# Performance work log

Hardware: AMD Instinct MI355X
Metric: run time of the kernel (lower is better)

Reference implementation:

```python
import jax, jax.numpy as jnp
import numpy as np

HEAD_DIM = 64  # config['head_dim']
# dropout_prob=0.1 is a no-op in eval mode; reference computes deterministic attention.

def setup_inputs() -> dict:
    key = jax.random.key(0)
    kq, kk, kv = jax.random.split(key, 3)
    shape = (2, 12, 2048, HEAD_DIM)  # [batch, heads, seq, head_dim]
    Q = jax.random.normal(kq, shape, dtype=jnp.float32)
    K = jax.random.normal(kk, shape, dtype=jnp.float32)
    V = jax.random.normal(kv, shape, dtype=jnp.float32)
    return {"Q": Q, "K": K, "V": V}

def reference(Q, K, V):
    # dot = Q @ K^T / sqrt(head_dim); attn = softmax(dot); X = attn @ V
    scale = 1.0 / np.float32(np.sqrt(HEAD_DIM))
    dot = jnp.einsum('bhqd,bhkd->bhqk', Q, K) * scale  # [B,H,S,S]
    attn = jax.nn.softmax(dot, axis=-1)
    X = jnp.einsum('bhqk,bhkd->bhqd', attn, V)
    return X
```

## Files before the change

kernel.cpp:

```cpp
#include <hip/hip_runtime.h>
#include <hip/hip_bf16.h>

typedef __attribute__((ext_vector_type(8))) short bf16x8;
typedef __attribute__((ext_vector_type(4))) float f32x4;
typedef __attribute__((ext_vector_type(4))) unsigned short u16x4;
typedef __attribute__((ext_vector_type(2))) unsigned int u32x2;
typedef __attribute__((ext_vector_type(4))) unsigned int u32x4;
typedef __attribute__((ext_vector_type(4))) _Float16 f16x4;
typedef __attribute__((ext_vector_type(8))) _Float16 f16x8;
typedef __attribute__((ext_vector_type(2))) __fp16 h16x2;
typedef __attribute__((ext_vector_type(4))) __fp16 h16x4;

#define SEQ 2048
#define HD 64
#define BH 24

__device__ __forceinline__ unsigned bfpack(float a, float b) {
  union { float f; unsigned u; } ua, ub; ua.f = a; ub.f = b;
  return __builtin_amdgcn_perm(ub.u + 0x8000u, ua.u + 0x8000u, 0x07060302u);
}
__device__ __forceinline__ unsigned short f2bf(float f) {
  union { float f; unsigned u; } v; v.f = f;
  unsigned r = v.u + 0x7fffu + ((v.u >> 16) & 1u);
  return (unsigned short)(r >> 16);
}

__global__ __launch_bounds__(256) void prep_kv(const float* __restrict__ K,
                                               const float* __restrict__ V,
                                               unsigned* __restrict__ Kb,
                                               _Float16* __restrict__ Vt) {
  __shared__ _Float16 t[64 * 68];
  const int bh = blockIdx.y;
  const int k0 = blockIdx.x * 64;
  const int tid = threadIdx.x;

  const float4* ks = (const float4*)(K + ((size_t)bh * SEQ + k0) * HD);
  unsigned* kd = Kb + ((size_t)bh * SEQ + k0) * (HD / 2);
#pragma unroll
  for (int i = 0; i < 4; ++i) {
    int f = tid + i * 256;
    float4 v = ks[f];
    u32x2 o;
    o.x = bfpack(v.x, v.y);
    o.y = bfpack(v.z, v.w);
    *(u32x2*)&kd[f * 2] = o;
  }

  const float4* vs = (const float4*)(V + ((size_t)bh * SEQ + k0) * HD);
#pragma unroll
  for (int i = 0; i < 4; ++i) {
    int f = tid + i * 256;
    int k = f >> 4, cg = f & 15;
    float4 v = vs[k * 16 + cg];
    int dg = cg * 4;
    t[(dg + 0) * 68 + k] = (_Float16)v.x;
    t[(dg + 1) * 68 + k] = (_Float16)v.y;
    t[(dg + 2) * 68 + k] = (_Float16)v.z;
    t[(dg + 3) * 68 + k] = (_Float16)v.w;
  }
  __syncthreads();
  int d = tid >> 2, kg = (tid & 3) * 16;
  _Float16* g = Vt + ((size_t)(bh * 64 + d)) * SEQ + k0 + (kg & 32) + ((kg >> 4) & 1) * 4;
#pragma unroll
  for (int r = 0; r < 4; ++r) {
    f16x4 x = *(f16x4*)&t[d * 68 + kg + r * 4];
    *(f16x4*)&g[r * 8] = x;
  }
}

__global__ __launch_bounds__(128) void attn_main(const float* __restrict__ Q,
                                                 const unsigned short* __restrict__ Kb,
                                                 const _Float16* __restrict__ Vt,
                                                 float* __restrict__ O) {
  __shared__ unsigned short kv[2][8192];

  const int tid  = threadIdx.x;
  const int lane = tid & 63;
  const int wv   = tid >> 6;
  const int quad = lane >> 4;
  const int n    = lane & 15;

  const int bh = blockIdx.x;
  const int q0 = blockIdx.y * 64;

  const float qscale = 0.125f * 1.44269504088896f;

  bf16x8 qf[2][2];
#pragma unroll
  for (int u = 0; u < 2; ++u) {
    const float* qb = Q + ((size_t)bh * SEQ + q0 + wv * 32 + u * 16 + n) * HD;
#pragma unroll
    for (int h = 0; h < 2; ++h) {
      float4 a = *(const float4*)(qb + h * 32 + quad * 8);
      float4 b = *(const float4*)(qb + h * 32 + quad * 8 + 4);
      u32x4 pk;
      pk.x = bfpack(a.x * qscale, a.y * qscale);
      pk.y = bfpack(a.z * qscale, a.w * qscale);
      pk.z = bfpack(b.x * qscale, b.y * qscale);
      pk.w = bfpack(b.z * qscale, b.w * qscale);
      qf[u][h] = __builtin_bit_cast(bf16x8, pk);
    }
  }

  const unsigned short* Kbase = Kb + (size_t)bh * SEQ * HD;
  const unsigned short* Vbase = (const unsigned short*)(Vt + (size_t)bh * HD * SEQ);
  const unsigned short* ksrc[4];
  const unsigned short* vsrc[4];
  int soff[4];
#pragma unroll
  for (int i = 0; i < 4; ++i) {
    int s = i * 128 + tid;
    int r = s >> 3, p = s & 7, G = p ^ (r & 7);
    ksrc[i] = Kbase + r * HD + G * 8;
    vsrc[i] = Vbase + (size_t)r * SEQ + G * 8;
    soff[i] = s * 8;
  }

#define DMA(it_)                                                                          \
  {                                                                                       \
    unsigned short* db_ = &kv[(it_) & 1][0];                                              \
    _Pragma("unroll")                                                                     \
    for (int i_ = 0; i_ < 4; ++i_) {                                                      \
      __builtin_amdgcn_global_load_lds(                                                   \
          (const __attribute__((address_space(1))) void*)(ksrc[i_] + (size_t)(it_) * 4096), \
          (__attribute__((address_space(3))) void*)(db_ + soff[i_]), 16, 0, 0);           \
      __builtin_amdgcn_global_load_lds(                                                   \
          (const __attribute__((address_space(1))) void*)(vsrc[i_] + (size_t)(it_) * 64), \
          (__attribute__((address_space(3))) void*)(db_ + 4096 + soff[i_]), 16, 0, 0);    \
    }                                                                                     \
  }

  f32x4 o[2][4] = {{{0,0,0,0},{0,0,0,0},{0,0,0,0},{0,0,0,0}},
                   {{0,0,0,0},{0,0,0,0},{0,0,0,0},{0,0,0,0}}};
  float lsum[2] = {0.f, 0.f};

  int ro[2];
#pragma unroll
  for (int h = 0; h < 2; ++h) ro[h] = n * 64 + (((h * 4 + quad) ^ (n & 7)) * 8);

  DMA(0);

  for (int it = 0; it < 32; ++it) {
    __syncthreads();
    if (it + 1 < 32) DMA(it + 1);

    const unsigned short* kb = &kv[it & 1][0];
    const unsigned short* vb = kb + 4096;

    f32x4 s[2][4] = {{{0,0,0,0},{0,0,0,0},{0,0,0,0},{0,0,0,0}},
                     {{0,0,0,0},{0,0,0,0},{0,0,0,0},{0,0,0,0}}};
#pragma unroll
    for (int t = 0; t < 4; ++t) {
#pragma unroll
      for (int h = 0; h < 2; ++h) {
        bf16x8 a = *(const bf16x8*)&kb[t * 1024 + ro[h]];
#pragma unroll
        for (int u = 0; u < 2; ++u)
          s[u][t] = __builtin_amdgcn_mfma_f32_16x16x32_bf16(a, qf[u][h], s[u][t], 0, 0, 0);
      }
    }

    f16x4 pf[2][4];
#pragma unroll
    for (int u = 0; u < 2; ++u) {
#pragma unroll
      for (int c = 0; c < 4; ++c) {
        float e0 = __builtin_amdgcn_exp2f(s[u][c][0]);
        float e1 = __builtin_amdgcn_exp2f(s[u][c][1]);
        float e2 = __builtin_amdgcn_exp2f(s[u][c][2]);
        float e3 = __builtin_amdgcn_exp2f(s[u][c][3]);
        lsum[u] += (e0 + e1) + (e2 + e3);
        h16x2 a_ = __builtin_amdgcn_cvt_pkrtz(e0, e1);
        h16x2 b_ = __builtin_amdgcn_cvt_pkrtz(e2, e3);
        h16x4 ab_ = __builtin_shufflevector(a_, b_, 0, 1, 2, 3);
        pf[u][c] = __builtin_bit_cast(f16x4, ab_);
      }
    }

#pragma unroll
    for (int t = 0; t < 4; ++t) {
#pragma unroll
      for (int h = 0; h < 2; ++h) {
        f16x8 v8 = *(const f16x8*)((const _Float16*)&vb[t * 1024 + ro[h]]);
        f16x4 vlo = __builtin_shufflevector(v8, v8, 0, 1, 2, 3);
        f16x4 vhi = __builtin_shufflevector(v8, v8, 4, 5, 6, 7);
#pragma unroll
        for (int u = 0; u < 2; ++u) {
          o[u][t] = __builtin_amdgcn_mfma_f32_16x16x16f16(vlo, pf[u][2 * h], o[u][t], 0, 0, 0);
          o[u][t] = __builtin_amdgcn_mfma_f32_16x16x16f16(vhi, pf[u][2 * h + 1], o[u][t], 0, 0, 0);
        }
      }
    }
  }
#undef DMA

#pragma unroll
  for (int u = 0; u < 2; ++u) {
    float l = lsum[u];
    l += __shfl_xor(l, 16);
    l += __shfl_xor(l, 32);
    float inv = 1.0f / l;
    float* og = O + ((size_t)bh * SEQ + q0 + wv * 32 + u * 16 + n) * HD + quad * 4;
#pragma unroll
    for (int t = 0; t < 4; ++t) {
      f32x4 r = o[u][t];
      r.x *= inv; r.y *= inv; r.z *= inv; r.w *= inv;
      *(f32x4*)(og + t * 16) = r;
    }
  }
}

#define F_QT 128
#define F_KT 64
#define F_LD 72

__global__ __launch_bounds__(512) void attn_fwd(const float* __restrict__ Q,
                                                const float* __restrict__ K,
                                                const float* __restrict__ V,
                                                float* __restrict__ O) {
  __shared__ unsigned short sm[(F_QT + F_KT + HD + 8 * 16) * F_LD];
  unsigned short* Qs = sm;
  unsigned short* Ks = Qs + F_QT * F_LD;
  unsigned short* Vt = Ks + F_KT * F_LD;
  unsigned short* Ps = Vt + HD * F_LD;

  const int tid = threadIdx.x, lane = tid & 63, wv = tid >> 6;
  const int quad = lane >> 4, n = lane & 15;
  const int bh = blockIdx.y, q0 = blockIdx.x * F_QT;
  const float* Qg = Q + ((size_t)bh * SEQ + q0) * HD;
  const float* Kg = K + (size_t)bh * SEQ * HD;
  const float* Vg = V + (size_t)bh * SEQ * HD;
  float* Og = O + ((size_t)bh * SEQ + q0) * HD;
  const float qscale = 0.125f * 1.44269504088896f;

#pragma unroll
  for (int i = 0; i < 4; ++i) {
    int f = tid + i * 512;
    int row = f >> 4, cg = f & 15;
    float4 qv = ((const float4*)Qg)[row * 16 + cg];
    u16x4 h;
    h.x = f2bf(qv.x * qscale); h.y = f2bf(qv.y * qscale);
    h.z = f2bf(qv.z * qscale); h.w = f2bf(qv.w * qscale);
    *(u16x4*)&Qs[row * F_LD + cg * 4] = h;
  }
  __syncthreads();
  bf16x8 qf0 = *(const bf16x8*)&Qs[(wv * 16 + n) * F_LD + quad * 8];
  bf16x8 qf1 = *(const bf16x8*)&Qs[(wv * 16 + n) * F_LD + 32 + quad * 8];
  f32x4 o[4] = {{0,0,0,0},{0,0,0,0},{0,0,0,0},{0,0,0,0}};
  float mrow[4] = {-1e30f,-1e30f,-1e30f,-1e30f};
  float lrow[4] = {0.f,0.f,0.f,0.f};
  unsigned short* Pw = Ps + wv * 16 * F_LD;

  for (int it = 0; it < SEQ / F_KT; ++it) {
    __syncthreads();
    const float* Ktg = Kg + (size_t)it * F_KT * HD;
    const float* Vtg = Vg + (size_t)it * F_KT * HD;
#pragma unroll
    for (int i = 0; i < 2; ++i) {
      int f = tid + i * 512;
      int row = f >> 4, cg = f & 15;
      float4 kvv = ((const float4*)Ktg)[row * 16 + cg];
      u16x4 hk;
      hk.x = f2bf(kvv.x); hk.y = f2bf(kvv.y); hk.z = f2bf(kvv.z); hk.w = f2bf(kvv.w);
      *(u16x4*)&Ks[row * F_LD + cg * 4] = hk;
      float4 vv = ((const float4*)Vtg)[row * 16 + cg];
      Vt[(cg * 4 + 0) * F_LD + row] = f2bf(vv.x);
      Vt[(cg * 4 + 1) * F_LD + row] = f2bf(vv.y);
      Vt[(cg * 4 + 2) * F_LD + row] = f2bf(vv.z);
      Vt[(cg * 4 + 3) * F_LD + row] = f2bf(vv.w);
    }
    __syncthreads();
    f32x4 s[4];
#pragma unroll
    for (int t = 0; t < 4; ++t) {
      bf16x8 b0 = *(const bf16x8*)&Ks[(t * 16 + n) * F_LD + quad * 8];
      bf16x8 b1 = *(const bf16x8*)&Ks[(t * 16 + n) * F_LD + 32 + quad * 8];
      f32x4 c = {0,0,0,0};
      c = __builtin_amdgcn_mfma_f32_16x16x32_bf16(qf0, b0, c, 0, 0, 0);
      c = __builtin_amdgcn_mfma_f32_16x16x32_bf16(qf1, b1, c, 0, 0, 0);
      s[t] = c;
    }
    float mnew[4], alpha[4], rsum[4];
#pragma unroll
    for (int r = 0; r < 4; ++r) {
      float ml = fmaxf(fmaxf(s[0][r], s[1][r]), fmaxf(s[2][r], s[3][r]));
      ml = fmaxf(ml, __shfl_xor(ml, 1));
      ml = fmaxf(ml, __shfl_xor(ml, 2));
      ml = fmaxf(ml, __shfl_xor(ml, 4));
      ml = fmaxf(ml, __shfl_xor(ml, 8));
      mnew[r] = fmaxf(mrow[r], ml);
      alpha[r] = __builtin_amdgcn_exp2f(mrow[r] - mnew[r]);
      mrow[r] = mnew[r];
      rsum[r] = 0.f;
    }
#pragma unroll
    for (int t = 0; t < 4; ++t)
#pragma unroll
      for (int r = 0; r < 4; ++r) {
        float p = __builtin_amdgcn_exp2f(s[t][r] - mnew[r]);
        rsum[r] += p;
        Pw[(quad * 4 + r) * F_LD + t * 16 + n] = f2bf(p);
      }
#pragma unroll
    for (int r = 0; r < 4; ++r) {
      float rs = rsum[r];
      rs += __shfl_xor(rs, 1); rs += __shfl_xor(rs, 2);
      rs += __shfl_xor(rs, 4); rs += __shfl_xor(rs, 8);
      lrow[r] = lrow[r] * alpha[r] + rs;
      o[0][r] *= alpha[r]; o[1][r] *= alpha[r];
      o[2][r] *= alpha[r]; o[3][r] *= alpha[r];
    }
    asm volatile("s_waitcnt lgkmcnt(0)" ::: "memory");
    bf16x8 p0 = *(const bf16x8*)&Pw[n * F_LD + quad * 8];
    bf16x8 p1 = *(const bf16x8*)&Pw[n * F_LD + 32 + quad * 8];
#pragma unroll
    for (int t = 0; t < 4; ++t) {
      bf16x8 v0 = *(const bf16x8*)&Vt[(t * 16 + n) * F_LD + quad * 8];
      bf16x8 v1 = *(const bf16x8*)&Vt[(t * 16 + n) * F_LD + 32 + quad * 8];
      o[t] = __builtin_amdgcn_mfma_f32_16x16x32_bf16(p0, v0, o[t], 0, 0, 0);
      o[t] = __builtin_amdgcn_mfma_f32_16x16x32_bf16(p1, v1, o[t], 0, 0, 0);
    }
  }
  float inv[4];
#pragma unroll
  for (int r = 0; r < 4; ++r) inv[r] = 1.0f / lrow[r];
#pragma unroll
  for (int t = 0; t < 4; ++t)
#pragma unroll
    for (int r = 0; r < 4; ++r)
      Og[(wv * 16 + quad * 4 + r) * HD + t * 16 + n] = o[t][r] * inv[r];
}

extern "C" void kernel_launch(void* const* d_in, const int* in_sizes, int n_in,
                              void* d_out, int out_size, void* d_ws, size_t ws_size,
                              hipStream_t stream) {
  const float* Q = (const float*)d_in[0];
  const float* K = (const float*)d_in[1];
  const float* V = (const float*)d_in[2];
  float* O = (float*)d_out;

  const size_t mat = (size_t)BH * SEQ * HD;
  const size_t need = 2 * mat * sizeof(unsigned short);

  if (ws_size >= need) {
    unsigned short* Kb = (unsigned short*)d_ws;
    _Float16* Vt = (_Float16*)(Kb + mat);
    prep_kv<<<dim3(SEQ / 64, BH), 256, 0, stream>>>(K, V, (unsigned*)Kb, Vt);
    attn_main<<<dim3(BH, SEQ / 64), 128, 0, stream>>>(Q, Kb, Vt, O);
  } else {
    attn_fwd<<<dim3(SEQ / F_QT, BH), 512, 0, stream>>>(Q, K, V, O);
  }
}
```

Measured before the change: 136.0 us.

## Triple-buffer K/V LDS tiles with partial vmcnt waits for deeper prefetch

Grows the shared K/V staging from two to three buffers and prefetches two tiles ahead. The wait before each iteration drops from a full __syncthreads drain to an explicit s_waitcnt vmcnt(8) plus s_barrier, so the next tile's global-to-LDS loads stay in flight while the current tile is computed. The aim is to hide global load latency behind the MFMA and exp work. In exchange LDS per block rises from 32KB to 48KB, which may reduce how many blocks fit per CU. The hand-written waitcnt counting must also stay correct, and the last iteration, where no new loads are issued, is handled by draining to vmcnt(0).

```diff
diff --git a/kernel.cpp b/kernel.cpp
--- a/kernel.cpp
+++ b/kernel.cpp
@@ -72,7 +72,7 @@
                                                  const unsigned short* __restrict__ Kb,
                                                  const _Float16* __restrict__ Vt,
                                                  float* __restrict__ O) {
-  __shared__ unsigned short kv[2][8192];
+  __shared__ unsigned short kv[3][8192];
 
   const int tid  = threadIdx.x;
   const int lane = tid & 63;
@@ -116,9 +116,9 @@
     soff[i] = s * 8;
   }
 
-#define DMA(it_)                                                                          \
+#define DMA_TO(buf_, it_)                                                                 \
   {                                                                                       \
-    unsigned short* db_ = &kv[(it_) & 1][0];                                              \
+    unsigned short* db_ = &kv[buf_][0];                                                   \
     _Pragma("unroll")                                                                     \
     for (int i_ = 0; i_ < 4; ++i_) {                                                      \
       __builtin_amdgcn_global_load_lds(                                                   \
@@ -128,6 +128,7 @@
           (const __attribute__((address_space(1))) void*)(vsrc[i_] + (size_t)(it_) * 64), \
           (__attribute__((address_space(3))) void*)(db_ + 4096 + soff[i_]), 16, 0, 0);    \
     }                                                                                     \
+    asm volatile("" ::: "memory");                      \
   }
 
   f32x4 o[2][4] = {{{0,0,0,0},{0,0,0,0},{0,0,0,0},{0,0,0,0}},
@@ -138,61 +139,71 @@
 #pragma unroll
   for (int h = 0; h < 2; ++h) ro[h] = n * 64 + (((h * 4 + quad) ^ (n & 7)) * 8);
 
-  DMA(0);
-
-  for (int it = 0; it < 32; ++it) {
-    __syncthreads();
-    if (it + 1 < 32) DMA(it + 1);
-
-    const unsigned short* kb = &kv[it & 1][0];
-    const unsigned short* vb = kb + 4096;
-
-    f32x4 s[2][4] = {{{0,0,0,0},{0,0,0,0},{0,0,0,0},{0,0,0,0}},
-                     {{0,0,0,0},{0,0,0,0},{0,0,0,0},{0,0,0,0}}};
-#pragma unroll
-    for (int t = 0; t < 4; ++t) {
-#pragma unroll
-      for (int h = 0; h < 2; ++h) {
-        bf16x8 a = *(const bf16x8*)&kb[t * 1024 + ro[h]];
-#pragma unroll
-        for (int u = 0; u < 2; ++u)
-          s[u][t] = __builtin_amdgcn_mfma_f32_16x16x32_bf16(a, qf[u][h], s[u][t], 0, 0, 0);
-      }
-    }
-
-    f16x4 pf[2][4];
-#pragma unroll
-    for (int u = 0; u < 2; ++u) {
-#pragma unroll
-      for (int c = 0; c < 4; ++c) {
-        float e0 = __builtin_amdgcn_exp2f(s[u][c][0]);
-        float e1 = __builtin_amdgcn_exp2f(s[u][c][1]);
-        float e2 = __builtin_amdgcn_exp2f(s[u][c][2]);
-        float e3 = __builtin_amdgcn_exp2f(s[u][c][3]);
-        lsum[u] += (e0 + e1) + (e2 + e3);
-        h16x2 a_ = __builtin_amdgcn_cvt_pkrtz(e0, e1);
-        h16x2 b_ = __builtin_amdgcn_cvt_pkrtz(e2, e3);
-        h16x4 ab_ = __builtin_shufflevector(a_, b_, 0, 1, 2, 3);
-        pf[u][c] = __builtin_bit_cast(f16x4, ab_);
-      }
-    }
-
-#pragma unroll
-    for (int t = 0; t < 4; ++t) {
-#pragma unroll
-      for (int h = 0; h < 2; ++h) {
-        f16x8 v8 = *(const f16x8*)((const _Float16*)&vb[t * 1024 + ro[h]]);
-        f16x4 vlo = __builtin_shufflevector(v8, v8, 0, 1, 2, 3);
-        f16x4 vhi = __builtin_shufflevector(v8, v8, 4, 5, 6, 7);
-#pragma unroll
-        for (int u = 0; u < 2; ++u) {
-          o[u][t] = __builtin_amdgcn_mfma_f32_16x16x16f16(vlo, pf[u][2 * h], o[u][t], 0, 0, 0);
-          o[u][t] = __builtin_amdgcn_mfma_f32_16x16x16f16(vhi, pf[u][2 * h + 1], o[u][t], 0, 0, 0);
-        }
-      }
-    }
-  }
-#undef DMA
+#define COMPUTE(buf_)                                                                     \
+  {                                                                                       \
+    const unsigned short* kb = &kv[buf_][0];                                              \
+    const unsigned short* vb = kb + 4096;                                                 \
+    f32x4 s[2][4] = {{{0,0,0,0},{0,0,0,0},{0,0,0,0},{0,0,0,0}},                           \
+                     {{0,0,0,0},{0,0,0,0},{0,0,0,0},{0,0,0,0}}};                          \
+    _Pragma("unroll")                                                                     \
+    for (int t = 0; t < 4; ++t) {                                                         \
+      _Pragma("unroll")                                                                   \
+      for (int h = 0; h < 2; ++h) {                                                       \
+        bf16x8 a = *(const bf16x8*)&kb[t * 1024 + ro[h]];                                 \
+        _Pragma("unroll")                                                                 \
+        for (int u = 0; u < 2; ++u)                                                       \
+          s[u][t] = __builtin_amdgcn_mfma_f32_16x16x32_bf16(a, qf[u][h], s[u][t], 0, 0, 0); \
+      }                                                                                   \
+    }                                                                                     \
+    f16x4 pf[2][4];                                                                       \
+    _Pragma("unroll")                                                                     \
+    for (int u = 0; u < 2; ++u) {                                                         \
+      _Pragma("unroll")                                                                   \
+      for (int c = 0; c < 4; ++c) {                                                       \
+        float e0 = __builtin_amdgcn_exp2f(s[u][c][0]);                                    \
+        float e1 = __builtin_amdgcn_exp2f(s[u][c][1]);                                    \
+        float e2 = __builtin_amdgcn_exp2f(s[u][c][2]);                                    \
+        float e3 = __builtin_amdgcn_exp2f(s[u][c][3]);                                    \
+        lsum[u] += (e0 + e1) + (e2 + e3);                                                 \
+        h16x2 a_ = __builtin_amdgcn_cvt_pkrtz(e0, e1);                                    \
+        h16x2 b_ = __builtin_amdgcn_cvt_pkrtz(e2, e3);                                    \
+        h16x4 ab_ = __builtin_shufflevector(a_, b_, 0, 1, 2, 3);                          \
+        pf[u][c] = __builtin_bit_cast(f16x4, ab_);                                        \
+      }                                                                                   \
+    }                                                                                     \
+    _Pragma("unroll")                                                                     \
+    for (int t = 0; t < 4; ++t) {                                                         \
+      _Pragma("unroll")                                                                   \
+      for (int h = 0; h < 2; ++h) {                                                       \
+        f16x8 v8 = *(const f16x8*)((const _Float16*)&vb[t * 1024 + ro[h]]);               \
+        f16x4 vlo = __builtin_shufflevector(v8, v8, 0, 1, 2, 3);                          \
+        f16x4 vhi = __builtin_shufflevector(v8, v8, 4, 5, 6, 7);                          \
+        _Pragma("unroll")                                                                 \
+        for (int u = 0; u < 2; ++u) {                                                     \
+          o[u][t] = __builtin_amdgcn_mfma_f32_16x16x16f16(vlo, pf[u][2 * h], o[u][t], 0, 0, 0); \
+          o[u][t] = __builtin_amdgcn_mfma_f32_16x16x16f16(vhi, pf[u][2 * h + 1], o[u][t], 0, 0, 0); \
+        }                                                                                 \
+      }                                                                                   \
+    }                                                                                     \
+  }
+
+  DMA_TO(0, 0);
+  DMA_TO(1, 1);
+
+  int bc = 0;
+  int bd = 2;
+  for (int it = 0; it < 31; ++it) {
+    asm volatile("s_waitcnt vmcnt(8)\n\ts_barrier" ::: "memory");
+    if (it < 30) DMA_TO(bd, it + 2);
+    COMPUTE(bc);
+    bc = (bc == 2) ? 0 : bc + 1;
+    bd = (bd == 2) ? 0 : bd + 1;
+  }
+  asm volatile("s_waitcnt vmcnt(0)\n\ts_barrier" ::: "memory");
+  COMPUTE(bc);
+
+#undef DMA_TO
+#undef COMPUTE
 
 #pragma unroll
   for (int u = 0; u < 2; ++u) {
```

After: 126.7 us. 6.8% less time.
